# Kernel tuning notes

Hardware: AMD Instinct MI355X
Metric: run time of the kernel (lower is better)

The kernel has to match this reference:

```python
import jax, jax.numpy as jnp
import numpy as np

N_DIS = 5000
N_GEN = 20000
N = N_DIS + N_GEN
E = 400000
N_MIRNA = 2000
EMB = 128
HID = 64


def setup_inputs() -> dict:
    key = jax.random.key(0)
    ks = jax.random.split(key, 20)
    def g(k, shape, scale=0.05):
        return jax.random.normal(k, shape, dtype=jnp.float32) * scale
    return {
        'd_features': g(ks[0], (N_DIS, 383), 1.0),
        'g_features': g(ks[1], (N_GEN, 4395), 1.0),
        'miRNA_dis': jax.random.uniform(ks[2], (N_MIRNA, N_DIS), dtype=jnp.float32),
        'gene_dis': jax.random.uniform(ks[3], (N_GEN, N_DIS), dtype=jnp.float32),
        'Wd': g(ks[4], (383, EMB)),
        'bd': jnp.zeros((EMB,), jnp.float32),
        'Wg': g(ks[5], (4395, EMB)),
        'bg': jnp.zeros((EMB,), jnp.float32),
        'W1': g(ks[6], (N_MIRNA, EMB)),
        'W4': g(ks[7], (N_DIS, EMB)),
        'Ws1': g(ks[8], (EMB, HID)),
        'Wn1': g(ks[9], (EMB, HID)),
        'b1': jnp.zeros((HID,), jnp.float32),
        'Ws2': g(ks[10], (HID, HID)),
        'Wn2': g(ks[11], (HID, HID)),
        'b2': jnp.zeros((HID,), jnp.float32),
        'src': jax.random.randint(ks[12], (E,), 0, N, dtype=jnp.int32),
        'dst': jax.random.randint(ks[13], (E,), 0, N, dtype=jnp.int32),
    }


def _sage_mean(h, src, dst, Ws, Wn, b):
    # DGL SAGEConv 'mean': fc_self(h) + fc_neigh(mean over in-neighbors) + bias
    msg = h[src]                                            # [E, d] gather
    agg = jax.ops.segment_sum(msg, dst, num_segments=N)     # [N, d] scatter-add
    deg = jax.ops.segment_sum(jnp.ones((dst.shape[0],), h.dtype), dst, num_segments=N)
    neigh = agg / jnp.maximum(deg, 1.0)[:, None]            # mean (zero-deg -> 0)
    return h @ Ws + neigh @ Wn + b


def reference(d_features, g_features, miRNA_dis, gene_dis, Wd, bd, Wg, bg,
              W1, W4, Ws1, Wn1, b1, Ws2, Wn2, b2, src, dst):
    # CrossCompressUnit outputs used by forward: A2 = M1^T W1, B1 = M2 W4
    A2 = miRNA_dis.T @ W1          # [N_DIS, EMB]
    B1 = gene_dis @ W4             # [N_GEN, EMB]
    # Node embeddings (dropout is identity at inference; torch.no_grad block)
    h_dis = 0.9 * (d_features @ Wd + bd) + 0.1 * A2   # [N_DIS, EMB]
    h_gen = 0.9 * (g_features @ Wg + bg) + 0.1 * B1   # [N_GEN, EMB]
    h = jnp.concatenate([h_dis, h_gen], axis=0)        # [N, EMB]
    h = _sage_mean(h, src, dst, Ws1, Wn1, b1)          # [N, 64]
    h = jax.nn.relu(h)
    h = _sage_mean(h, src, dst, Ws2, Wn2, b2)          # [N, 64]
    return h
```

## Files before the change

kernel.cpp:

```cpp
#include <hip/hip_runtime.h>

#define NDIS 5000
#define NGEN 20000
#define NTOT 25000
#define EDG  400000

typedef __attribute__((ext_vector_type(8))) short short8;
typedef __attribute__((ext_vector_type(4))) float f32x4;
typedef __attribute__((ext_vector_type(4), aligned(4))) float f32x4u;

constexpr size_t AL(size_t x) { return (x + 255) & ~(size_t)255; }
constexpr size_t OFF_H0   = 0;
constexpr size_t OFF_PQ   = AL(OFF_H0  + (size_t)NTOT * 128 * 4);
constexpr size_t OFF_H1   = AL(OFF_PQ  + (size_t)NTOT * 128 * 4);
constexpr size_t OFF_DEG  = AL(OFF_H1  + (size_t)NTOT * 64 * 4);
constexpr size_t OFF_RS   = AL(OFF_DEG + (size_t)NTOT * 4);
constexpr size_t OFF_CUR  = AL(OFF_RS  + (size_t)(NTOT + 1) * 4);
constexpr size_t OFF_ESRC = AL(OFF_CUR + (size_t)NTOT * 4);
constexpr size_t OFF_MIT  = AL(OFF_ESRC + (size_t)EDG * 4);
constexpr size_t OFF_BDIS = AL(OFF_MIT + (size_t)5000 * 2016 * 2);
constexpr size_t OFF_BGEN = AL(OFF_BDIS + (size_t)128 * 2400 * 2);
constexpr size_t OFF_BS1  = AL(OFF_BGEN + (size_t)128 * 9440 * 2);
constexpr size_t OFF_BS2  = AL(OFF_BS1 + (size_t)128 * 128 * 2);

__device__ __forceinline__ ushort f2bf(float f) {
    unsigned u = __float_as_uint(f);
    u += 0x7fffu + ((u >> 16) & 1u);
    return (ushort)(u >> 16);
}

__device__ __forceinline__ void MFMA(f32x4& d, short8 a, short8 b) {
    asm volatile("v_mfma_f32_16x16x32_bf16 %0, %1, %2, %0"
                 : "+v"(d) : "v"(a), "v"(b));
}

struct TcvtIns { const float* p[9]; };

__global__ __launch_bounds__(256) void k_tcvt_multi(TcvtIns ins, char* ws)
{
    constexpr int   TRr[9] = {383, 2000, 4395, 5000, 2000, 128, 128, 64, 64};
    constexpr int   TCc[9] = {128, 128, 128, 128, 5000, 64, 64, 64, 64};
    constexpr int   TLD[9] = {2400, 2400, 9440, 9440, 2016, 128, 128, 64, 64};
    constexpr int   TRP[9] = {384, 2016, 4416, 5024, 2016, 128, 128, 64, 64};
    constexpr float TSC[9] = {0.9f, 0.1f, 0.9f, 0.1f, 1.f, 1.f, 1.f, 1.f, 1.f};
    constexpr size_t TOUT[9] = {OFF_BDIS, OFF_BDIS + 384 * 2, OFF_BGEN,
                                OFF_BGEN + (size_t)4416 * 2, OFF_MIT,
                                OFF_BS1, OFF_BS1 + (size_t)64 * 128 * 2,
                                OFF_BS2, OFF_BS2 + (size_t)64 * 64 * 2};
    constexpr int TNBX[9] = {4, 4, 4, 4, 157, 2, 2, 2, 2};
    constexpr int PRE[10] = {0, 48, 300, 852, 1480, 11371, 11379, 11387, 11391, 11395};

    int bid = blockIdx.x;
    int d = 0;
#pragma unroll
    for (int q = 1; q < 9; ++q) if (bid >= PRE[q]) d = q;
    int local = bid - PRE[d];
    int bx = local % TNBX[d], by = local / TNBX[d];
    const int R = TRr[d], C = TCc[d], ld = TLD[d], Rp = TRP[d];
    const float scale = TSC[d];
    const float* in = ins.p[d];
    ushort* out = (ushort*)(ws + TOUT[d]);

    __shared__ float t[32][33];
    int tx = threadIdx.x & 31, ty = threadIdx.x >> 5;
    int c0 = bx * 32, r0 = by * 32;
#pragma unroll
    for (int j = 0; j < 4; ++j) {
        int r = r0 + ty + j * 8, c = c0 + tx;
        t[ty + j * 8][tx] = (r < R && c < C) ? in[(size_t)r * C + c] : 0.f;
    }
    __syncthreads();
#pragma unroll
    for (int j = 0; j < 4; ++j) {
        int c = c0 + ty + j * 8, r = r0 + tx;
        if (c < C && r < Rp) out[(size_t)c * ld + r] = f2bf(scale * t[tx][ty + j * 8]);
    }
}

template<bool A2BF16, bool ATOMIC>
__global__ __launch_bounds__(256) void mfma_gemm(
    const float* __restrict__ A1, int lda1, int K1, int K1p,
    const void* __restrict__ A2, int lda2, int K2,
    const ushort* __restrict__ Bt, int ldB, int ktiles,
    float* __restrict__ C, int M, const float* __restrict__ bias)
{
    __shared__ ushort Alds[64 * 40];
    __shared__ ushort Blds[128 * 40];
    const int tid  = threadIdx.x;
    const int lane = tid & 63;
    const int w    = tid >> 6;
    const int wr = w >> 1, wc = w & 1;
    const int bm0 = blockIdx.x * 64;
    const int ar = tid >> 2, aq = tid & 3;
    const int br = tid >> 1, bh = tid & 1;

    const int per = (ktiles + gridDim.y - 1) / gridDim.y;
    const int kt0 = blockIdx.y * per;
    const int kt1 = min(ktiles, kt0 + per);
    if (kt0 >= kt1) return;

    f32x4 acc[2][4];
#pragma unroll
    for (int i = 0; i < 2; ++i)
#pragma unroll
        for (int j = 0; j < 4; ++j) acc[i][j] = {0.f, 0.f, 0.f, 0.f};

    const int arow = bm0 + ar;
    for (int kt = kt0; kt < kt1; ++kt) {
        const int kk = kt << 5;
        {
            short8 s = {0, 0, 0, 0, 0, 0, 0, 0};
            if (arow < M) {
                int k = kk + aq * 8;
                if (k < K1p) {
                    const float* p = A1 + (size_t)arow * lda1 + k;
                    if (k + 8 <= K1) {
                        f32x4u v0 = *(const f32x4u*)p;
                        f32x4u v1 = *(const f32x4u*)(p + 4);
#pragma unroll
                        for (int e = 0; e < 4; ++e) {
                            s[e]     = (short)f2bf(v0[e]);
                            s[4 + e] = (short)f2bf(v1[e]);
                        }
                    } else {
#pragma unroll
                        for (int e = 0; e < 8; ++e)
                            s[e] = (short)f2bf((k + e < K1) ? p[e] : 0.f);
                    }
                } else {
                    int kc = k - K1p;
                    if (A2BF16) {
                        s = *(const short8*)((const ushort*)A2 + (size_t)arow * lda2 + kc);
                    } else {
                        const float* p = (const float*)A2 + (size_t)arow * lda2 + kc;
                        if (kc + 8 <= K2) {
                            f32x4u v0 = *(const f32x4u*)p;
                            f32x4u v1 = *(const f32x4u*)(p + 4);
#pragma unroll
                            for (int e = 0; e < 4; ++e) {
                                s[e]     = (short)f2bf(v0[e]);
                                s[4 + e] = (short)f2bf(v1[e]);
                            }
                        } else {
#pragma unroll
                            for (int e = 0; e < 8; ++e)
                                s[e] = (short)f2bf((kc + e < K2) ? p[e] : 0.f);
                        }
                    }
                }
            }
            *(short8*)&Alds[ar * 40 + aq * 8] = s;
        }
        {
            const ushort* p = Bt + (size_t)br * ldB + kk + bh * 16;
            *(short8*)&Blds[br * 40 + bh * 16]     = *(const short8*)p;
            *(short8*)&Blds[br * 40 + bh * 16 + 8] = *(const short8*)(p + 8);
        }
        __syncthreads();
        {
            const int fr = lane & 15, kg = (lane >> 4) * 8;
            short8 a0 = *(const short8*)&Alds[(wr * 32 + fr) * 40 + kg];
            short8 a1 = *(const short8*)&Alds[(wr * 32 + 16 + fr) * 40 + kg];
            short8 b0 = *(const short8*)&Blds[(wc * 64 + fr) * 40 + kg];
            short8 b1 = *(const short8*)&Blds[(wc * 64 + 16 + fr) * 40 + kg];
            short8 b2 = *(const short8*)&Blds[(wc * 64 + 32 + fr) * 40 + kg];
            short8 b3 = *(const short8*)&Blds[(wc * 64 + 48 + fr) * 40 + kg];
            MFMA(acc[0][0], a0, b0); MFMA(acc[0][1], a0, b1);
            MFMA(acc[0][2], a0, b2); MFMA(acc[0][3], a0, b3);
            MFMA(acc[1][0], a1, b0); MFMA(acc[1][1], a1, b1);
            MFMA(acc[1][2], a1, b2); MFMA(acc[1][3], a1, b3);
        }
        __syncthreads();
    }
    asm volatile("s_nop 7\n\ts_nop 7\n\ts_nop 7" ::: "memory");
    const int fr = lane & 15, fq = lane >> 4;
#pragma unroll
    for (int mi = 0; mi < 2; ++mi)
#pragma unroll
        for (int ni = 0; ni < 4; ++ni)
#pragma unroll
            for (int r = 0; r < 4; ++r) {
                int row = bm0 + wr * 32 + mi * 16 + fq * 4 + r;
                if (row < M) {
                    int col = wc * 64 + ni * 16 + fr;
                    if (ATOMIC) {
                        atomicAdd(&C[(size_t)row * 128 + col], acc[mi][ni][r]);
                    } else {
                        float v = acc[mi][ni][r];
                        if (col < 64) v += bias[col];
                        C[(size_t)row * 128 + col] = v;
                    }
                }
            }
}

__global__ void k_binit(float* __restrict__ h0, const float* __restrict__ bd,
                        const float* __restrict__ bg) {
    int i = blockIdx.x * 256 + threadIdx.x;
    if (i >= NTOT * 128) return;
    int col = i & 127;
    h0[i] = 0.9f * ((i >> 7) < NDIS ? bd[col] : bg[col]);
}

__global__ void k_deg(const int* __restrict__ dst, int* __restrict__ deg, int E) {
    int e = blockIdx.x * blockDim.x + threadIdx.x;
    if (e < E) atomicAdd(&deg[dst[e]], 1);
}

__global__ __launch_bounds__(1024) void k_scan(const int* __restrict__ deg,
                                               int* __restrict__ row_start,
                                               int* __restrict__ cursor, int n) {
    __shared__ int wsum[16];
    __shared__ int carry_s;
    int t = threadIdx.x;
    int lane = t & 63, wid = t >> 6;
    if (t == 0) { carry_s = 0; row_start[0] = 0; }
    __syncthreads();
    for (int base = 0; base < n; base += 1024) {
        int i = base + t;
        int v = (i < n) ? deg[i] : 0;
        int x = v;
#pragma unroll
        for (int off = 1; off < 64; off <<= 1) {
            int y = __shfl_up(x, off, 64);
            if (lane >= off) x += y;
        }
        if (lane == 63) wsum[wid] = x;
        __syncthreads();
        if (wid == 0) {
            int s = (lane < 16) ? wsum[lane] : 0;
#pragma unroll
            for (int off = 1; off < 16; off <<= 1) {
                int y = __shfl_up(s, off, 64);
                if (lane >= off) s += y;
            }
            if (lane < 16) wsum[lane] = s;
        }
        __syncthreads();
        int pre = (wid > 0 ? wsum[wid - 1] : 0) + carry_s;
        int incl = x + pre;
        if (i < n) { row_start[i + 1] = incl; cursor[i] = incl - v; }
        __syncthreads();
        if (t == 1023) carry_s = incl;
        __syncthreads();
    }
}

__global__ void k_fill(const int* __restrict__ src, const int* __restrict__ dst,
                       int* __restrict__ cursor, int* __restrict__ esrc, int E) {
    int e = blockIdx.x * blockDim.x + threadIdx.x;
    if (e < E) {
        int pos = atomicAdd(&cursor[dst[e]], 1);
        esrc[pos] = src[e];
    }
}

__global__ __launch_bounds__(64) void k_agg(const float* __restrict__ PQ,
                                            const int* __restrict__ rs,
                                            const int* __restrict__ esrc,
                                            float* __restrict__ out, int relu)
{
    int n = blockIdx.x, t = threadIdx.x;
    int s0 = rs[n], s1 = rs[n + 1];
    float a0 = 0.f, a1 = 0.f, a2 = 0.f, a3 = 0.f;
    int i = s0;
    for (; i + 4 <= s1; i += 4) {
        int e0 = esrc[i], e1 = esrc[i + 1], e2 = esrc[i + 2], e3 = esrc[i + 3];
        a0 += PQ[(size_t)e0 * 128 + 64 + t];
        a1 += PQ[(size_t)e1 * 128 + 64 + t];
        a2 += PQ[(size_t)e2 * 128 + 64 + t];
        a3 += PQ[(size_t)e3 * 128 + 64 + t];
    }
    for (; i < s1; ++i) a0 += PQ[(size_t)esrc[i] * 128 + 64 + t];
    float s = (a0 + a1) + (a2 + a3);
    float dg = (float)(s1 - s0);
    s /= fmaxf(dg, 1.f);
    float v = PQ[(size_t)n * 128 + t] + s;
    if (relu) v = fmaxf(v, 0.f);
    out[(size_t)n * 64 + t] = v;
}

extern "C" void kernel_launch(void* const* d_in, const int* in_sizes, int n_in,
                              void* d_out, int out_size, void* d_ws, size_t ws_size,
                              hipStream_t stream)
{
    const float* d_features = (const float*)d_in[0];
    const float* g_features = (const float*)d_in[1];
    const float* miRNA_dis  = (const float*)d_in[2];
    const float* gene_dis   = (const float*)d_in[3];
    const float* Wd  = (const float*)d_in[4];
    const float* bd  = (const float*)d_in[5];
    const float* Wg  = (const float*)d_in[6];
    const float* bg  = (const float*)d_in[7];
    const float* W1  = (const float*)d_in[8];
    const float* W4  = (const float*)d_in[9];
    const float* Ws1 = (const float*)d_in[10];
    const float* Wn1 = (const float*)d_in[11];
    const float* b1  = (const float*)d_in[12];
    const float* Ws2 = (const float*)d_in[13];
    const float* Wn2 = (const float*)d_in[14];
    const float* b2  = (const float*)d_in[15];
    const int* src = (const int*)d_in[16];
    const int* dst = (const int*)d_in[17];
    (void)in_sizes; (void)n_in; (void)out_size; (void)ws_size;

    char* ws = (char*)d_ws;
    float*  h0   = (float*)(ws + OFF_H0);
    float*  PQ   = (float*)(ws + OFF_PQ);
    float*  h1   = (float*)(ws + OFF_H1);
    int*    deg  = (int*)(ws + OFF_DEG);
    int*    rs   = (int*)(ws + OFF_RS);
    int*    cur  = (int*)(ws + OFF_CUR);
    int*    esrc = (int*)(ws + OFF_ESRC);
    ushort* miT  = (ushort*)(ws + OFF_MIT);
    ushort* Bdis = (ushort*)(ws + OFF_BDIS);
    ushort* Bgen = (ushort*)(ws + OFF_BGEN);
    ushort* Bs1  = (ushort*)(ws + OFF_BS1);
    ushort* Bs2  = (ushort*)(ws + OFF_BS2);

    hipMemsetAsync(deg, 0, (size_t)NTOT * 4, stream);
    k_deg<<<(EDG + 255) / 256, 256, 0, stream>>>(dst, deg, EDG);
    k_scan<<<1, 1024, 0, stream>>>(deg, rs, cur, NTOT);
    k_fill<<<(EDG + 255) / 256, 256, 0, stream>>>(src, dst, cur, esrc, EDG);

    TcvtIns ins;
    ins.p[0] = Wd;  ins.p[1] = W1;  ins.p[2] = Wg;  ins.p[3] = W4;
    ins.p[4] = miRNA_dis; ins.p[5] = Ws1; ins.p[6] = Wn1; ins.p[7] = Ws2; ins.p[8] = Wn2;
    k_tcvt_multi<<<11395, 256, 0, stream>>>(ins, ws);

    k_binit<<<(NTOT * 128 + 255) / 256, 256, 0, stream>>>(h0, bd, bg);
    mfma_gemm<true, true><<<dim3(79, 4), 256, 0, stream>>>(
        d_features, 383, 383, 384, miT, 2016, 2016, Bdis, 2400, 75, h0, NDIS, nullptr);
    mfma_gemm<false, true><<<dim3(313, 4), 256, 0, stream>>>(
        g_features, 4395, 4395, 4416, gene_dis, 5000, 5000, Bgen, 9440, 295,
        h0 + (size_t)NDIS * 128, NGEN, nullptr);

    mfma_gemm<false, false><<<dim3(391, 1), 256, 0, stream>>>(
        h0, 128, 128, 128, nullptr, 0, 0, Bs1, 128, 4, PQ, NTOT, b1);
    k_agg<<<NTOT, 64, 0, stream>>>(PQ, rs, esrc, h1, 1);

    mfma_gemm<false, false><<<dim3(391, 1), 256, 0, stream>>>(
        h1, 64, 64, 64, nullptr, 0, 0, Bs2, 64, 2, PQ, NTOT, b2);
    k_agg<<<NTOT, 64, 0, stream>>>(PQ, rs, esrc, (float*)d_out, 0);
}
```

Baseline: 426.1 us.

## Double-buffer GEMM global loads in registers and widen K tile to 64

Measured after the change: 410.7 us. 1.04x faster.

```diff
diff --git a/kernel.cpp b/kernel.cpp
--- a/kernel.cpp
+++ b/kernel.cpp
@@ -18,9 +18,9 @@
 constexpr size_t OFF_CUR  = AL(OFF_RS  + (size_t)(NTOT + 1) * 4);
 constexpr size_t OFF_ESRC = AL(OFF_CUR + (size_t)NTOT * 4);
 constexpr size_t OFF_MIT  = AL(OFF_ESRC + (size_t)EDG * 4);
-constexpr size_t OFF_BDIS = AL(OFF_MIT + (size_t)5000 * 2016 * 2);
-constexpr size_t OFF_BGEN = AL(OFF_BDIS + (size_t)128 * 2400 * 2);
-constexpr size_t OFF_BS1  = AL(OFF_BGEN + (size_t)128 * 9440 * 2);
+constexpr size_t OFF_BDIS = AL(OFF_MIT + (size_t)5000 * 2048 * 2);
+constexpr size_t OFF_BGEN = AL(OFF_BDIS + (size_t)128 * 2432 * 2);
+constexpr size_t OFF_BS1  = AL(OFF_BGEN + (size_t)128 * 9472 * 2);
 constexpr size_t OFF_BS2  = AL(OFF_BS1 + (size_t)128 * 128 * 2);
 
 __device__ __forceinline__ ushort f2bf(float f) {
@@ -40,15 +40,15 @@
 {
     constexpr int   TRr[9] = {383, 2000, 4395, 5000, 2000, 128, 128, 64, 64};
     constexpr int   TCc[9] = {128, 128, 128, 128, 5000, 64, 64, 64, 64};
-    constexpr int   TLD[9] = {2400, 2400, 9440, 9440, 2016, 128, 128, 64, 64};
-    constexpr int   TRP[9] = {384, 2016, 4416, 5024, 2016, 128, 128, 64, 64};
+    constexpr int   TLD[9] = {2432, 2432, 9472, 9472, 2048, 128, 128, 64, 64};
+    constexpr int   TRP[9] = {384, 2048, 4416, 5056, 2048, 128, 128, 64, 64};
     constexpr float TSC[9] = {0.9f, 0.1f, 0.9f, 0.1f, 1.f, 1.f, 1.f, 1.f, 1.f};
-    constexpr size_t TOUT[9] = {OFF_BDIS, OFF_BDIS + 384 * 2, OFF_BGEN,
+    constexpr size_t TOUT[9] = {OFF_BDIS, OFF_BDIS + (size_t)384 * 2, OFF_BGEN,
                                 OFF_BGEN + (size_t)4416 * 2, OFF_MIT,
                                 OFF_BS1, OFF_BS1 + (size_t)64 * 128 * 2,
                                 OFF_BS2, OFF_BS2 + (size_t)64 * 64 * 2};
     constexpr int TNBX[9] = {4, 4, 4, 4, 157, 2, 2, 2, 2};
-    constexpr int PRE[10] = {0, 48, 300, 852, 1480, 11371, 11379, 11387, 11391, 11395};
+    constexpr int PRE[10] = {0, 48, 304, 856, 1488, 11536, 11544, 11552, 11556, 11560};
 
     int bid = blockIdx.x;
     int d = 0;
@@ -84,15 +84,15 @@
     const ushort* __restrict__ Bt, int ldB, int ktiles,
     float* __restrict__ C, int M, const float* __restrict__ bias)
 {
-    __shared__ ushort Alds[64 * 40];
-    __shared__ ushort Blds[128 * 40];
+    __shared__ ushort Alds[64 * 72];
+    __shared__ ushort Blds[128 * 72];
     const int tid  = threadIdx.x;
     const int lane = tid & 63;
     const int w    = tid >> 6;
     const int wr = w >> 1, wc = w & 1;
     const int bm0 = blockIdx.x * 64;
-    const int ar = tid >> 2, aq = tid & 3;
-    const int br = tid >> 1, bh = tid & 1;
+    const int ar = tid >> 2, aks = (tid & 3) * 16;
+    const int br = tid >> 1, bks = (tid & 1) * 32;
 
     const int per = (ktiles + gridDim.y - 1) / gridDim.y;
     const int kt0 = blockIdx.y * per;
@@ -106,72 +106,108 @@
         for (int j = 0; j < 4; ++j) acc[i][j] = {0.f, 0.f, 0.f, 0.f};
 
     const int arow = bm0 + ar;
-    for (int kt = kt0; kt < kt1; ++kt) {
-        const int kk = kt << 5;
-        {
-            short8 s = {0, 0, 0, 0, 0, 0, 0, 0};
-            if (arow < M) {
-                int k = kk + aq * 8;
-                if (k < K1p) {
-                    const float* p = A1 + (size_t)arow * lda1 + k;
-                    if (k + 8 <= K1) {
+
+    float  fa0[16], fa1[16];
+    short8 sa0[2],  sa1[2];
+    short8 sb0[4],  sb1[4];
+
+    auto loadA = [&](int kt, float* fa, short8* sa) {
+        if (arow >= M) return;
+        const int kkb = kt << 6;
+#pragma unroll
+        for (int s = 0; s < 2; ++s) {
+            const int k = kkb + aks + s * 8;
+            if (k < K1p) {
+                const float* p = A1 + (size_t)arow * lda1 + k;
+                if (k + 8 <= K1) {
+                    f32x4u v0 = *(const f32x4u*)p;
+                    f32x4u v1 = *(const f32x4u*)(p + 4);
+#pragma unroll
+                    for (int e = 0; e < 4; ++e) { fa[s*8+e] = v0[e]; fa[s*8+4+e] = v1[e]; }
+                } else {
+#pragma unroll
+                    for (int e = 0; e < 8; ++e) fa[s*8+e] = (k + e < K1) ? p[e] : 0.f;
+                }
+            } else {
+                const int kc = k - K1p;
+                if (A2BF16) {
+                    sa[s] = *(const short8*)((const ushort*)A2 + (size_t)arow * lda2 + kc);
+                } else {
+                    const float* p = (const float*)A2 + (size_t)arow * lda2 + kc;
+                    if (kc + 8 <= K2) {
                         f32x4u v0 = *(const f32x4u*)p;
                         f32x4u v1 = *(const f32x4u*)(p + 4);
 #pragma unroll
-                        for (int e = 0; e < 4; ++e) {
-                            s[e]     = (short)f2bf(v0[e]);
-                            s[4 + e] = (short)f2bf(v1[e]);
-                        }
+                        for (int e = 0; e < 4; ++e) { fa[s*8+e] = v0[e]; fa[s*8+4+e] = v1[e]; }
                     } else {
 #pragma unroll
-                        for (int e = 0; e < 8; ++e)
-                            s[e] = (short)f2bf((k + e < K1) ? p[e] : 0.f);
-                    }
-                } else {
-                    int kc = k - K1p;
-                    if (A2BF16) {
-                        s = *(const short8*)((const ushort*)A2 + (size_t)arow * lda2 + kc);
-                    } else {
-                        const float* p = (const float*)A2 + (size_t)arow * lda2 + kc;
-                        if (kc + 8 <= K2) {
-                            f32x4u v0 = *(const f32x4u*)p;
-                            f32x4u v1 = *(const f32x4u*)(p + 4);
-#pragma unroll
-                            for (int e = 0; e < 4; ++e) {
-                                s[e]     = (short)f2bf(v0[e]);
-                                s[4 + e] = (short)f2bf(v1[e]);
-                            }
-                        } else {
-#pragma unroll
-                            for (int e = 0; e < 8; ++e)
-                                s[e] = (short)f2bf((kc + e < K2) ? p[e] : 0.f);
-                        }
+                        for (int e = 0; e < 8; ++e) fa[s*8+e] = (kc + e < K2) ? p[e] : 0.f;
                     }
                 }
             }
-            *(short8*)&Alds[ar * 40 + aq * 8] = s;
-        }
-        {
-            const ushort* p = Bt + (size_t)br * ldB + kk + bh * 16;
-            *(short8*)&Blds[br * 40 + bh * 16]     = *(const short8*)p;
-            *(short8*)&Blds[br * 40 + bh * 16 + 8] = *(const short8*)(p + 8);
-        }
-        __syncthreads();
-        {
-            const int fr = lane & 15, kg = (lane >> 4) * 8;
-            short8 a0 = *(const short8*)&Alds[(wr * 32 + fr) * 40 + kg];
-            short8 a1 = *(const short8*)&Alds[(wr * 32 + 16 + fr) * 40 + kg];
-            short8 b0 = *(const short8*)&Blds[(wc * 64 + fr) * 40 + kg];
-            short8 b1 = *(const short8*)&Blds[(wc * 64 + 16 + fr) * 40 + kg];
-            short8 b2 = *(const short8*)&Blds[(wc * 64 + 32 + fr) * 40 + kg];
-            short8 b3 = *(const short8*)&Blds[(wc * 64 + 48 + fr) * 40 + kg];
+        }
+    };
+    auto loadB = [&](int kt, short8* sb) {
+        const ushort* p = Bt + (size_t)br * ldB + (kt << 6) + bks;
+#pragma unroll
+        for (int s = 0; s < 4; ++s) sb[s] = *(const short8*)(p + s * 8);
+    };
+    auto writeT = [&](int kt, const float* fa, const short8* sa, const short8* sb) {
+        const int kkb = kt << 6;
+#pragma unroll
+        for (int s = 0; s < 2; ++s) {
+            short8 v;
+            if (A2BF16 && (kkb + aks + s * 8) >= K1p) {
+                v = sa[s];
+            } else {
+#pragma unroll
+                for (int e = 0; e < 8; ++e) v[e] = (short)f2bf(fa[s * 8 + e]);
+            }
+            *(short8*)&Alds[ar * 72 + aks + s * 8] = v;
+        }
+#pragma unroll
+        for (int s = 0; s < 4; ++s)
+            *(short8*)&Blds[br * 72 + bks + s * 8] = sb[s];
+    };
+    auto compute = [&]() {
+        const int fr = lane & 15;
+        const int kq = (lane >> 4) * 8;
+#pragma unroll
+        for (int ks2 = 0; ks2 < 2; ++ks2) {
+            const int ko = ks2 * 32 + kq;
+            short8 a0 = *(const short8*)&Alds[(wr * 32 +      fr) * 72 + ko];
+            short8 a1 = *(const short8*)&Alds[(wr * 32 + 16 + fr) * 72 + ko];
+            short8 b0 = *(const short8*)&Blds[(wc * 64 +      fr) * 72 + ko];
+            short8 b1 = *(const short8*)&Blds[(wc * 64 + 16 + fr) * 72 + ko];
+            short8 b2 = *(const short8*)&Blds[(wc * 64 + 32 + fr) * 72 + ko];
+            short8 b3 = *(const short8*)&Blds[(wc * 64 + 48 + fr) * 72 + ko];
             MFMA(acc[0][0], a0, b0); MFMA(acc[0][1], a0, b1);
             MFMA(acc[0][2], a0, b2); MFMA(acc[0][3], a0, b3);
             MFMA(acc[1][0], a1, b0); MFMA(acc[1][1], a1, b1);
             MFMA(acc[1][2], a1, b2); MFMA(acc[1][3], a1, b3);
         }
-        __syncthreads();
-    }
+    };
+
+    loadA(kt0, fa0, sa0); loadB(kt0, sb0);
+    int kt = kt0;
+    while (true) {
+        __builtin_amdgcn_s_barrier();
+        writeT(kt, fa0, sa0, sb0);
+        if (kt + 1 < kt1) { loadA(kt + 1, fa1, sa1); loadB(kt + 1, sb1); }
+        asm volatile("s_waitcnt lgkmcnt(0)" ::: "memory");
+        __builtin_amdgcn_s_barrier();
+        compute();
+        if (++kt >= kt1) break;
+
+        __builtin_amdgcn_s_barrier();
+        writeT(kt, fa1, sa1, sb1);
+        if (kt + 1 < kt1) { loadA(kt + 1, fa0, sa0); loadB(kt + 1, sb0); }
+        asm volatile("s_waitcnt lgkmcnt(0)" ::: "memory");
+        __builtin_amdgcn_s_barrier();
+        compute();
+        if (++kt >= kt1) break;
+    }
+
     asm volatile("s_nop 7\n\ts_nop 7\n\ts_nop 7" ::: "memory");
     const int fr = lane & 15, fq = lane >> 4;
 #pragma unroll
@@ -326,20 +362,20 @@
     TcvtIns ins;
     ins.p[0] = Wd;  ins.p[1] = W1;  ins.p[2] = Wg;  ins.p[3] = W4;
     ins.p[4] = miRNA_dis; ins.p[5] = Ws1; ins.p[6] = Wn1; ins.p[7] = Ws2; ins.p[8] = Wn2;
-    k_tcvt_multi<<<11395, 256, 0, stream>>>(ins, ws);
+    k_tcvt_multi<<<11560, 256, 0, stream>>>(ins, ws);
 
     k_binit<<<(NTOT * 128 + 255) / 256, 256, 0, stream>>>(h0, bd, bg);
     mfma_gemm<true, true><<<dim3(79, 4), 256, 0, stream>>>(
-        d_features, 383, 383, 384, miT, 2016, 2016, Bdis, 2400, 75, h0, NDIS, nullptr);
+        d_features, 383, 383, 384, miT, 2048, 2048, Bdis, 2432, 38, h0, NDIS, nullptr);
     mfma_gemm<false, true><<<dim3(313, 4), 256, 0, stream>>>(
-        g_features, 4395, 4395, 4416, gene_dis, 5000, 5000, Bgen, 9440, 295,
+        g_features, 4395, 4395, 4416, gene_dis, 5000, 5000, Bgen, 9472, 148,
         h0 + (size_t)NDIS * 128, NGEN, nullptr);
 
     mfma_gemm<false, false><<<dim3(391, 1), 256, 0, stream>>>(
-        h0, 128, 128, 128, nullptr, 0, 0, Bs1, 128, 4, PQ, NTOT, b1);
+        h0, 128, 128, 128, nullptr, 0, 0, Bs1, 128, 2, PQ, NTOT, b1);
     k_agg<<<NTOT, 64, 0, stream>>>(PQ, rs, esrc, h1, 1);
 
     mfma_gemm<false, false><<<dim3(391, 1), 256, 0, stream>>>(
-        h1, 64, 64, 64, nullptr, 0, 0, Bs2, 64, 2, PQ, NTOT, b2);
+        h1, 64, 64, 64, nullptr, 0, 0, Bs2, 64, 1, PQ, NTOT, b2);
     k_agg<<<NTOT, 64, 0, stream>>>(PQ, rs, esrc, (float*)d_out, 0);
 }
```

## Replace LDS-tiled GEMM with single-wave register GEMM using pre-fragmented B layout

Applied to the files above, without the earlier changes.

After: 472.8 us. 1.11x slower.

```diff
diff --git a/kernel.cpp b/kernel.cpp
--- a/kernel.cpp
+++ b/kernel.cpp
@@ -8,6 +8,7 @@
 typedef __attribute__((ext_vector_type(8))) short short8;
 typedef __attribute__((ext_vector_type(4))) float f32x4;
 typedef __attribute__((ext_vector_type(4), aligned(4))) float f32x4u;
+typedef __attribute__((ext_vector_type(4))) unsigned int uint4v;
 
 constexpr size_t AL(size_t x) { return (x + 255) & ~(size_t)255; }
 constexpr size_t OFF_H0   = 0;
@@ -18,9 +19,11 @@
 constexpr size_t OFF_CUR  = AL(OFF_RS  + (size_t)(NTOT + 1) * 4);
 constexpr size_t OFF_ESRC = AL(OFF_CUR + (size_t)NTOT * 4);
 constexpr size_t OFF_MIT  = AL(OFF_ESRC + (size_t)EDG * 4);
-constexpr size_t OFF_BDIS = AL(OFF_MIT + (size_t)5000 * 2016 * 2);
-constexpr size_t OFF_BGEN = AL(OFF_BDIS + (size_t)128 * 2400 * 2);
-constexpr size_t OFF_BS1  = AL(OFF_BGEN + (size_t)128 * 9440 * 2);
+constexpr size_t OFF_BWD  = AL(OFF_MIT + (size_t)5000 * 2048 * 2);
+constexpr size_t OFF_BW1  = AL(OFF_BWD + (size_t)128 * 384 * 2);
+constexpr size_t OFF_BWG  = AL(OFF_BW1 + (size_t)128 * 2048 * 2);
+constexpr size_t OFF_BW4  = AL(OFF_BWG + (size_t)128 * 4416 * 2);
+constexpr size_t OFF_BS1  = AL(OFF_BW4 + (size_t)128 * 5056 * 2);
 constexpr size_t OFF_BS2  = AL(OFF_BS1 + (size_t)128 * 128 * 2);
 
 __device__ __forceinline__ ushort f2bf(float f) {
@@ -29,6 +32,12 @@
     return (ushort)(u >> 16);
 }
 
+__device__ __forceinline__ unsigned cvtpk(float a, float b) {
+    unsigned r;
+    asm("v_cvt_pk_bf16_f32 %0, %1, %2" : "=v"(r) : "v"(a), "v"(b));
+    return r;
+}
+
 __device__ __forceinline__ void MFMA(f32x4& d, short8 a, short8 b) {
     asm volatile("v_mfma_f32_16x16x32_bf16 %0, %1, %2, %0"
                  : "+v"(d) : "v"(a), "v"(b));
@@ -38,17 +47,17 @@
 
 __global__ __launch_bounds__(256) void k_tcvt_multi(TcvtIns ins, char* ws)
 {
-    constexpr int   TRr[9] = {383, 2000, 4395, 5000, 2000, 128, 128, 64, 64};
-    constexpr int   TCc[9] = {128, 128, 128, 128, 5000, 64, 64, 64, 64};
-    constexpr int   TLD[9] = {2400, 2400, 9440, 9440, 2016, 128, 128, 64, 64};
-    constexpr int   TRP[9] = {384, 2016, 4416, 5024, 2016, 128, 128, 64, 64};
-    constexpr float TSC[9] = {0.9f, 0.1f, 0.9f, 0.1f, 1.f, 1.f, 1.f, 1.f, 1.f};
-    constexpr size_t TOUT[9] = {OFF_BDIS, OFF_BDIS + 384 * 2, OFF_BGEN,
-                                OFF_BGEN + (size_t)4416 * 2, OFF_MIT,
-                                OFF_BS1, OFF_BS1 + (size_t)64 * 128 * 2,
-                                OFF_BS2, OFF_BS2 + (size_t)64 * 64 * 2};
-    constexpr int TNBX[9] = {4, 4, 4, 4, 157, 2, 2, 2, 2};
-    constexpr int PRE[10] = {0, 48, 300, 852, 1480, 11371, 11379, 11387, 11391, 11395};
+    constexpr int   TR[9]   = {383, 2000, 4395, 5000, 2000, 128, 128, 64, 64};
+    constexpr int   TC[9]   = {128, 128, 128, 128, 5000, 64, 64, 64, 64};
+    constexpr int   TKT[9]  = {12, 64, 138, 158, 2048 , 4, 4, 2, 2};
+    constexpr int   TRP[9]  = {384, 2048, 4416, 5056, 2048, 128, 128, 64, 64};
+    constexpr int   TNOFF[9]= {0, 0, 0, 0, 0, 0, 64, 0, 64};
+    constexpr int   TMODE[9]= {1, 1, 1, 1, 0, 1, 1, 1, 1};
+    constexpr float TSC[9]  = {0.9f, 0.1f, 0.9f, 0.1f, 1.f, 1.f, 1.f, 1.f, 1.f};
+    constexpr size_t TOUT[9]= {OFF_BWD, OFF_BW1, OFF_BWG, OFF_BW4, OFF_MIT,
+                               OFF_BS1, OFF_BS1, OFF_BS2, OFF_BS2};
+    constexpr int TNBX[9]   = {4, 4, 4, 4, 157, 2, 2, 2, 2};
+    constexpr int PRE[10]   = {0, 48, 304, 856, 1488, 11536, 11544, 11552, 11556, 11560};
 
     int bid = blockIdx.x;
     int d = 0;
@@ -56,7 +65,7 @@
     for (int q = 1; q < 9; ++q) if (bid >= PRE[q]) d = q;
     int local = bid - PRE[d];
     int bx = local % TNBX[d], by = local / TNBX[d];
-    const int R = TRr[d], C = TCc[d], ld = TLD[d], Rp = TRP[d];
+    const int R = TR[d], C = TC[d], KT = TKT[d], Rp = TRP[d], noff = TNOFF[d];
     const float scale = TSC[d];
     const float* in = ins.p[d];
     ushort* out = (ushort*)(ws + TOUT[d]);
@@ -73,120 +82,120 @@
 #pragma unroll
     for (int j = 0; j < 4; ++j) {
         int c = c0 + ty + j * 8, r = r0 + tx;
-        if (c < C && r < Rp) out[(size_t)c * ld + r] = f2bf(scale * t[tx][ty + j * 8]);
-    }
-}
-
-template<bool A2BF16, bool ATOMIC>
-__global__ __launch_bounds__(256) void mfma_gemm(
-    const float* __restrict__ A1, int lda1, int K1, int K1p,
-    const void* __restrict__ A2, int lda2, int K2,
-    const ushort* __restrict__ Bt, int ldB, int ktiles,
+        if (c >= C || r >= Rp) continue;
+        ushort bv = f2bf(scale * t[tx][ty + j * 8]);
+        if (TMODE[d] == 0) {
+            out[(size_t)c * KT + r] = bv;
+        } else {
+            int n = noff + c, k = r;
+            out[(size_t)((n >> 4) * KT + (k >> 5)) * 512 +
+                (((k >> 3) & 3) * 16 + (n & 15)) * 8 + (k & 7)] = bv;
+        }
+    }
+}
+
+template<bool ABF16, bool ATOMIC>
+__global__ __launch_bounds__(64) void gemm_bf(
+    const void* __restrict__ Av, int lda, int K1,
+    const ushort* __restrict__ Bf, int KT,
     float* __restrict__ C, int M, const float* __restrict__ bias)
 {
-    __shared__ ushort Alds[64 * 40];
-    __shared__ ushort Blds[128 * 40];
-    const int tid  = threadIdx.x;
-    const int lane = tid & 63;
-    const int w    = tid >> 6;
-    const int wr = w >> 1, wc = w & 1;
-    const int bm0 = blockIdx.x * 64;
-    const int ar = tid >> 2, aq = tid & 3;
-    const int br = tid >> 1, bh = tid & 1;
-
-    const int per = (ktiles + gridDim.y - 1) / gridDim.y;
+    const int lane = threadIdx.x;
+    const int fr = lane & 15, kq = lane >> 4;
+    const int mb = blockIdx.x * 32;
+    const int r0 = min(mb + fr, M - 1);
+    const int r1 = min(mb + 16 + fr, M - 1);
+    const int per = (KT + gridDim.y - 1) / gridDim.y;
     const int kt0 = blockIdx.y * per;
-    const int kt1 = min(ktiles, kt0 + per);
+    const int kt1 = min(KT, kt0 + per);
     if (kt0 >= kt1) return;
 
-    f32x4 acc[2][4];
+    f32x4 acc[2][8];
 #pragma unroll
     for (int i = 0; i < 2; ++i)
 #pragma unroll
-        for (int j = 0; j < 4; ++j) acc[i][j] = {0.f, 0.f, 0.f, 0.f};
-
-    const int arow = bm0 + ar;
-    for (int kt = kt0; kt < kt1; ++kt) {
-        const int kk = kt << 5;
-        {
-            short8 s = {0, 0, 0, 0, 0, 0, 0, 0};
-            if (arow < M) {
-                int k = kk + aq * 8;
-                if (k < K1p) {
-                    const float* p = A1 + (size_t)arow * lda1 + k;
-                    if (k + 8 <= K1) {
-                        f32x4u v0 = *(const f32x4u*)p;
-                        f32x4u v1 = *(const f32x4u*)(p + 4);
-#pragma unroll
-                        for (int e = 0; e < 4; ++e) {
-                            s[e]     = (short)f2bf(v0[e]);
-                            s[4 + e] = (short)f2bf(v1[e]);
-                        }
-                    } else {
-#pragma unroll
-                        for (int e = 0; e < 8; ++e)
-                            s[e] = (short)f2bf((k + e < K1) ? p[e] : 0.f);
-                    }
-                } else {
-                    int kc = k - K1p;
-                    if (A2BF16) {
-                        s = *(const short8*)((const ushort*)A2 + (size_t)arow * lda2 + kc);
-                    } else {
-                        const float* p = (const float*)A2 + (size_t)arow * lda2 + kc;
-                        if (kc + 8 <= K2) {
-                            f32x4u v0 = *(const f32x4u*)p;
-                            f32x4u v1 = *(const f32x4u*)(p + 4);
-#pragma unroll
-                            for (int e = 0; e < 4; ++e) {
-                                s[e]     = (short)f2bf(v0[e]);
-                                s[4 + e] = (short)f2bf(v1[e]);
-                            }
-                        } else {
-#pragma unroll
-                            for (int e = 0; e < 8; ++e)
-                                s[e] = (short)f2bf((kc + e < K2) ? p[e] : 0.f);
-                        }
-                    }
+        for (int j = 0; j < 8; ++j) acc[i][j] = {0.f, 0.f, 0.f, 0.f};
+
+    float  fa0[2][8], fa1[2][8];
+    short8 sb0[8], sb1[8];
+
+    auto loadA = [&](int kt, float (&fa)[2][8]) {
+        const int kb = kt * 32 + kq * 8;
+        if (ABF16) {
+            const ushort* A = (const ushort*)Av;
+            *(short8*)&fa[0][0] = *(const short8*)(A + (size_t)r0 * lda + kb);
+            *(short8*)&fa[1][0] = *(const short8*)(A + (size_t)r1 * lda + kb);
+        } else {
+            const float* A = (const float*)Av;
+            if (kt * 32 + 32 <= K1) {
+                const float* p0 = A + (size_t)r0 * lda + kb;
+                const float* p1 = A + (size_t)r1 * lda + kb;
+                *(f32x4u*)&fa[0][0] = *(const f32x4u*)p0;
+                *(f32x4u*)&fa[0][4] = *(const f32x4u*)(p0 + 4);
+                *(f32x4u*)&fa[1][0] = *(const f32x4u*)p1;
+                *(f32x4u*)&fa[1][4] = *(const f32x4u*)(p1 + 4);
+            } else {
+#pragma unroll
+                for (int e = 0; e < 8; ++e) {
+                    const int kk = kb + e;
+                    const bool ok = kk < K1;
+                    fa[0][e] = ok ? A[(size_t)r0 * lda + kk] : 0.f;
+                    fa[1][e] = ok ? A[(size_t)r1 * lda + kk] : 0.f;
                 }
             }
-            *(short8*)&Alds[ar * 40 + aq * 8] = s;
-        }
-        {
-            const ushort* p = Bt + (size_t)br * ldB + kk + bh * 16;
-            *(short8*)&Blds[br * 40 + bh * 16]     = *(const short8*)p;
-            *(short8*)&Blds[br * 40 + bh * 16 + 8] = *(const short8*)(p + 8);
-        }
-        __syncthreads();
-        {
-            const int fr = lane & 15, kg = (lane >> 4) * 8;
-            short8 a0 = *(const short8*)&Alds[(wr * 32 + fr) * 40 + kg];
-            short8 a1 = *(const short8*)&Alds[(wr * 32 + 16 + fr) * 40 + kg];
-            short8 b0 = *(const short8*)&Blds[(wc * 64 + fr) * 40 + kg];
-            short8 b1 = *(const short8*)&Blds[(wc * 64 + 16 + fr) * 40 + kg];
-            short8 b2 = *(const short8*)&Blds[(wc * 64 + 32 + fr) * 40 + kg];
-            short8 b3 = *(const short8*)&Blds[(wc * 64 + 48 + fr) * 40 + kg];
-            MFMA(acc[0][0], a0, b0); MFMA(acc[0][1], a0, b1);
-            MFMA(acc[0][2], a0, b2); MFMA(acc[0][3], a0, b3);
-            MFMA(acc[1][0], a1, b0); MFMA(acc[1][1], a1, b1);
-            MFMA(acc[1][2], a1, b2); MFMA(acc[1][3], a1, b3);
-        }
-        __syncthreads();
-    }
+        }
+    };
+    auto loadB = [&](int kt, short8 (&sb)[8]) {
+#pragma unroll
+        for (int nt = 0; nt < 8; ++nt)
+            sb[nt] = *(const short8*)(Bf + (size_t)(nt * KT + kt) * 512 + lane * 8);
+    };
+    auto comp = [&](float (&fa)[2][8], short8 (&sb)[8]) {
+        short8 a0, a1;
+        if (ABF16) {
+            a0 = *(const short8*)&fa[0][0];
+            a1 = *(const short8*)&fa[1][0];
+        } else {
+            uint4v u0 = {cvtpk(fa[0][0], fa[0][1]), cvtpk(fa[0][2], fa[0][3]),
+                         cvtpk(fa[0][4], fa[0][5]), cvtpk(fa[0][6], fa[0][7])};
+            uint4v u1 = {cvtpk(fa[1][0], fa[1][1]), cvtpk(fa[1][2], fa[1][3]),
+                         cvtpk(fa[1][4], fa[1][5]), cvtpk(fa[1][6], fa[1][7])};
+            a0 = __builtin_bit_cast(short8, u0);
+            a1 = __builtin_bit_cast(short8, u1);
+        }
+#pragma unroll
+        for (int nt = 0; nt < 8; ++nt) {
+            MFMA(acc[0][nt], a0, sb[nt]);
+            MFMA(acc[1][nt], a1, sb[nt]);
+        }
+    };
+
+    loadA(kt0, fa0); loadB(kt0, sb0);
+    if (kt0 + 1 < kt1) { loadA(kt0 + 1, fa1); loadB(kt0 + 1, sb1); }
+    int kt = kt0;
+    while (true) {
+        comp(fa0, sb0);
+        if (++kt >= kt1) break;
+        if (kt + 1 < kt1) { loadA(kt + 1, fa0); loadB(kt + 1, sb0); }
+        comp(fa1, sb1);
+        if (++kt >= kt1) break;
+        if (kt + 1 < kt1) { loadA(kt + 1, fa1); loadB(kt + 1, sb1); }
+    }
+
     asm volatile("s_nop 7\n\ts_nop 7\n\ts_nop 7" ::: "memory");
-    const int fr = lane & 15, fq = lane >> 4;
-#pragma unroll
-    for (int mi = 0; mi < 2; ++mi)
-#pragma unroll
-        for (int ni = 0; ni < 4; ++ni)
+#pragma unroll
+    for (int mt = 0; mt < 2; ++mt)
+#pragma unroll
+        for (int nt = 0; nt < 8; ++nt)
 #pragma unroll
             for (int r = 0; r < 4; ++r) {
-                int row = bm0 + wr * 32 + mi * 16 + fq * 4 + r;
+                int row = mb + mt * 16 + kq * 4 + r;
                 if (row < M) {
-                    int col = wc * 64 + ni * 16 + fr;
+                    int col = nt * 16 + fr;
                     if (ATOMIC) {
-                        atomicAdd(&C[(size_t)row * 128 + col], acc[mi][ni][r]);
+                        atomicAdd(&C[(size_t)row * 128 + col], acc[mt][nt][r]);
                     } else {
-                        float v = acc[mi][ni][r];
+                        float v = acc[mt][nt][r];
                         if (col < 64) v += bias[col];
                         C[(size_t)row * 128 + col] = v;
                     }
@@ -313,8 +322,10 @@
     int*    cur  = (int*)(ws + OFF_CUR);
     int*    esrc = (int*)(ws + OFF_ESRC);
     ushort* miT  = (ushort*)(ws + OFF_MIT);
-    ushort* Bdis = (ushort*)(ws + OFF_BDIS);
-    ushort* Bgen = (ushort*)(ws + OFF_BGEN);
+    ushort* Bwd  = (ushort*)(ws + OFF_BWD);
+    ushort* Bw1  = (ushort*)(ws + OFF_BW1);
+    ushort* Bwg  = (ushort*)(ws + OFF_BWG);
+    ushort* Bw4  = (ushort*)(ws + OFF_BW4);
     ushort* Bs1  = (ushort*)(ws + OFF_BS1);
     ushort* Bs2  = (ushort*)(ws + OFF_BS2);
 
@@ -326,20 +337,23 @@
     TcvtIns ins;
     ins.p[0] = Wd;  ins.p[1] = W1;  ins.p[2] = Wg;  ins.p[3] = W4;
     ins.p[4] = miRNA_dis; ins.p[5] = Ws1; ins.p[6] = Wn1; ins.p[7] = Ws2; ins.p[8] = Wn2;
-    k_tcvt_multi<<<11395, 256, 0, stream>>>(ins, ws);
+    k_tcvt_multi<<<11560, 256, 0, stream>>>(ins, ws);
 
     k_binit<<<(NTOT * 128 + 255) / 256, 256, 0, stream>>>(h0, bd, bg);
-    mfma_gemm<true, true><<<dim3(79, 4), 256, 0, stream>>>(
-        d_features, 383, 383, 384, miT, 2016, 2016, Bdis, 2400, 75, h0, NDIS, nullptr);
-    mfma_gemm<false, true><<<dim3(313, 4), 256, 0, stream>>>(
-        g_features, 4395, 4395, 4416, gene_dis, 5000, 5000, Bgen, 9440, 295,
-        h0 + (size_t)NDIS * 128, NGEN, nullptr);
-
-    mfma_gemm<false, false><<<dim3(391, 1), 256, 0, stream>>>(
-        h0, 128, 128, 128, nullptr, 0, 0, Bs1, 128, 4, PQ, NTOT, b1);
+    gemm_bf<false, true><<<dim3(157, 2), 64, 0, stream>>>(
+        d_features, 383, 383, Bwd, 12, h0, NDIS, nullptr);
+    gemm_bf<true, true><<<dim3(157, 4), 64, 0, stream>>>(
+        miT, 2048, 2048, Bw1, 64, h0, NDIS, nullptr);
+    gemm_bf<false, true><<<dim3(625, 3), 64, 0, stream>>>(
+        g_features, 4395, 4395, Bwg, 138, h0 + (size_t)NDIS * 128, NGEN, nullptr);
+    gemm_bf<false, true><<<dim3(625, 3), 64, 0, stream>>>(
+        gene_dis, 5000, 5000, Bw4, 158, h0 + (size_t)NDIS * 128, NGEN, nullptr);
+
+    gemm_bf<false, false><<<dim3(782, 1), 64, 0, stream>>>(
+        h0, 128, 128, Bs1, 4, PQ, NTOT, b1);
     k_agg<<<NTOT, 64, 0, stream>>>(PQ, rs, esrc, h1, 1);
 
-    mfma_gemm<false, false><<<dim3(391, 1), 256, 0, stream>>>(
-        h1, 64, 64, 64, nullptr, 0, 0, Bs2, 64, 2, PQ, NTOT, b2);
+    gemm_bf<false, false><<<dim3(782, 1), 64, 0, stream>>>(
+        h1, 64, 64, Bs2, 2, PQ, NTOT, b2);
     k_agg<<<NTOT, 64, 0, stream>>>(PQ, rs, esrc, (float*)d_out, 0);
 }
```
